# Optimization experiments

Hardware: AMD Instinct MI355X
Metric: run time of the kernel (lower is better)

The kernel has to match this reference:

```python
import jax, jax.numpy as jnp
import numpy as np

NUM_HEADS = 8
DIM_HEAD = 48
SCALE = DIM_HEAD ** -0.5


def setup_inputs() -> dict:
    key = jax.random.key(0)
    k1, k2, k3 = jax.random.split(key, 3)
    B, N, D = 4, 2048, 384
    inner = NUM_HEADS * DIM_HEAD  # 384
    x = jax.random.normal(k1, (B, N, D), dtype=jnp.float32)
    # store weights in [in, out] layout (equivalent to torch Linear W.T)
    Wqkv = jax.random.normal(k2, (D, 3 * inner), dtype=jnp.float32) * (D ** -0.5)
    Wproj = jax.random.normal(k3, (inner, D), dtype=jnp.float32) * (inner ** -0.5)
    bproj = jnp.zeros((D,), dtype=jnp.float32)
    return {"x": x, "Wqkv": Wqkv, "Wproj": Wproj, "bproj": bproj}


def reference(x, Wqkv, Wproj, bproj):
    B, N, D = x.shape
    h, dh = NUM_HEADS, DIM_HEAD
    C = h * dh
    # fused QKV projection (qkv_bias=False)
    qkv = (x @ Wqkv).reshape(B, N, 3, h, dh)
    q = qkv[:, :, 0].transpose(0, 2, 1, 3)  # [B, h, N, dh]
    k = qkv[:, :, 1].transpose(0, 2, 1, 3)
    v = qkv[:, :, 2].transpose(0, 2, 1, 3)
    # naive attention: materialize [B, h, N, N] scores
    sim = jnp.einsum("bhqd,bhkd->bhqk", q, k) * SCALE
    attn = jax.nn.softmax(sim, axis=-1)
    out = jnp.einsum("bhqk,bhkd->bhqd", attn, v)  # [B, h, N, dh]
    out = out.transpose(0, 2, 1, 3).reshape(B, N, C)
    return out @ Wproj + bproj
```

## Files before the change

### kernel.cpp

```cpp
#include <hip/hip_runtime.h>
#include <hip/hip_bf16.h>


typedef _Float16 f16x8 __attribute__((ext_vector_type(8)));
typedef _Float16 f16x4 __attribute__((ext_vector_type(4)));
typedef float    f32x4 __attribute__((ext_vector_type(4)));
typedef float    f32x16 __attribute__((ext_vector_type(16)));

#define QSCL 0.20822035963448658f

__global__ __launch_bounds__(256) void prep(const float4* __restrict__ x,
                                            const float* __restrict__ wq,
                                            const float* __restrict__ wp,
                                            f16x4* __restrict__ xh4,
                                            _Float16* __restrict__ wqt,
                                            _Float16* __restrict__ wpt)
{
    __shared__ _Float16 t[64][65];
    const int blk = blockIdx.x, tid = threadIdx.x;
    if (blk < 144) {
        const float* src; _Float16* dst; int Nn, k0, n0;
        if (blk < 108) {
            src = wq; dst = wqt; Nn = 1152;
            k0 = (blk % 6) * 64; n0 = (blk / 6) * 64;
        } else {
            const int b2 = blk - 108;
            src = wp; dst = wpt; Nn = 384;
            k0 = (b2 % 6) * 64; n0 = (b2 / 6) * 64;
        }
        #pragma unroll
        for (int i = 0; i < 16; i++) {
            const int id = tid + i * 256;
            const int k = id >> 6, n = id & 63;
            t[k][n] = (_Float16)src[(size_t)(k0 + k) * Nn + n0 + n];
        }
        __syncthreads();
        #pragma unroll
        for (int i = 0; i < 16; i++) {
            const int id = tid + i * 256;
            const int n = id >> 6, k = id & 63;
            dst[(size_t)(n0 + n) * 384 + k0 + k] = t[k][n];
        }
    } else {
        const int base = (blk - 144) * 3072;
        #pragma unroll
        for (int r = 0; r < 12; r++) {
            const int j = base + r * 256 + tid;
            const float4 tt = x[j];
            f16x4 h;
            h[0] = (_Float16)tt.x; h[1] = (_Float16)tt.y;
            h[2] = (_Float16)tt.z; h[3] = (_Float16)tt.w;
            xh4[j] = h;
        }
    }
}

__global__ __launch_bounds__(256) void qkv_f16(const _Float16* __restrict__ A,
                                               const _Float16* __restrict__ Bt,
                                               _Float16* __restrict__ qh,
                                               _Float16* __restrict__ kh,
                                               _Float16* __restrict__ vt)
{
    __shared__ _Float16 As[128][72];
    __shared__ _Float16 Bs[64][72];
    const int tid = threadIdx.x;
    const int w = tid >> 6, lane = tid & 63, cl = lane & 15, quad = lane >> 4;
    const int bm = blockIdx.x, bn = blockIdx.y;

    f32x4 acc[2][4];
    const f32x4 z4 = {0.f, 0.f, 0.f, 0.f};
    #pragma unroll
    for (int mi = 0; mi < 2; mi++)
        #pragma unroll
        for (int t = 0; t < 4; t++) acc[mi][t] = z4;

    const int ar = tid >> 3, ac = (tid & 7) * 8;
    const _Float16* Ag = A  + (size_t)(bm * 128 + ar) * 384 + ac;
    const _Float16* Bg = Bt + (size_t)(bn * 64  + ar) * 384 + ac;

    f16x8 pa[4], pb[2];
    #pragma unroll
    for (int j = 0; j < 4; j++) pa[j] = *(const f16x8*)(Ag + (size_t)(32 * j) * 384);
    #pragma unroll
    for (int j = 0; j < 2; j++) pb[j] = *(const f16x8*)(Bg + (size_t)(32 * j) * 384);

    for (int k0 = 0; k0 < 384; k0 += 64) {
        __syncthreads();
        #pragma unroll
        for (int j = 0; j < 4; j++) *(f16x8*)&As[ar + 32 * j][ac] = pa[j];
        #pragma unroll
        for (int j = 0; j < 2; j++) *(f16x8*)&Bs[ar + 32 * j][ac] = pb[j];
        __syncthreads();
        if (k0 + 64 < 384) {
            #pragma unroll
            for (int j = 0; j < 4; j++)
                pa[j] = *(const f16x8*)(Ag + (size_t)(32 * j) * 384 + k0 + 64);
            #pragma unroll
            for (int j = 0; j < 2; j++)
                pb[j] = *(const f16x8*)(Bg + (size_t)(32 * j) * 384 + k0 + 64);
        }
        #pragma unroll
        for (int kh2 = 0; kh2 < 2; kh2++) {
            f16x8 bf[4];
            #pragma unroll
            for (int t = 0; t < 4; t++)
                bf[t] = *(const f16x8*)&Bs[t * 16 + cl][kh2 * 32 + quad * 8];
            #pragma unroll
            for (int mi = 0; mi < 2; mi++) {
                const f16x8 af = *(const f16x8*)&As[w * 32 + mi * 16 + cl][kh2 * 32 + quad * 8];
                #pragma unroll
                for (int t = 0; t < 4; t++)
                    acc[mi][t] = __builtin_amdgcn_mfma_f32_16x16x32_f16(af, bf[t], acc[mi][t], 0, 0, 0);
            }
        }
    }

    const int s = (bn * 64) / 384;
    #pragma unroll
    for (int t = 0; t < 4; t++) {
        const int col  = bn * 64 + t * 16 + cl - s * 384;
        const int head = col / 48, d = col - head * 48;
        #pragma unroll
        for (int mi = 0; mi < 2; mi++) {
            #pragma unroll
            for (int r = 0; r < 4; r++) {
                const int row = bm * 128 + w * 32 + mi * 16 + quad * 4 + r;
                const int b = row >> 11, n = row & 2047;
                const int bh = b * 8 + head;
                const float v = acc[mi][t][r];
                if (s == 0)
                    qh[(size_t)(bh * 2048 + n) * 48 + d] = (_Float16)(v * QSCL);
                else if (s == 1)
                    kh[(size_t)(bh * 2048 + n) * 48 + d] = (_Float16)v;
                else
                    vt[(size_t)(bh * 48 + d) * 2048 + n] = (_Float16)v;
            }
        }
    }
}

__global__ __launch_bounds__(256) void attn_f16(const _Float16* __restrict__ qh,
                                                const _Float16* __restrict__ kh,
                                                const _Float16* __restrict__ vt,
                                                _Float16* __restrict__ ab)
{
    __shared__ _Float16 Ks[64][56];
    __shared__ _Float16 Vts[64][72];
    __shared__ _Float16 Ps[128][72];
    const int tid = threadIdx.x;
    const int w = tid >> 6, lane = tid & 63, ln = lane & 31, h = lane >> 5;
    const int bh = blockIdx.x, qt = blockIdx.y;

    for (int i = tid; i < 16 * 72; i += 256) {
        const int r = 48 + i / 72, c = i - (i / 72) * 72;
        Vts[r][c] = (r == 48) ? (_Float16)1.0f : (_Float16)0.0f;
    }

    f16x8 qf[3];
    {
        const _Float16* qp = qh + (size_t)(bh * 2048 + qt * 128 + w * 32 + ln) * 48 + 8 * h;
        qf[0] = *(const f16x8*)qp;
        qf[1] = *(const f16x8*)(qp + 16);
        qf[2] = *(const f16x8*)(qp + 32);
    }

    f32x16 o0, o1;
    #pragma unroll
    for (int r = 0; r < 16; r++) { o0[r] = 0.f; o1[r] = 0.f; }

    const _Float16* kbase = kh + (size_t)bh * 2048 * 48;
    const _Float16* vbase = vt + (size_t)bh * 48 * 2048;

    const int kr0 = tid / 6,         kc0 = (tid % 6) * 8;
    const int kid1 = tid + 256;
    const int kr1 = kid1 / 6,        kc1 = (kid1 % 6) * 8;
    const int vr0 = tid >> 3,        vc0 = (tid & 7) * 8;
    const int vr1 = (tid + 256) >> 3;
    const _Float16* ks0 = kbase + (size_t)kr0 * 48 + kc0;
    const _Float16* ks1 = kbase + (size_t)kr1 * 48 + kc1;
    const _Float16* vs0 = vbase + (size_t)vr0 * 2048 + vc0;
    const _Float16* vs1 = vbase + (size_t)vr1 * 2048 + vc0;

    f16x8 rk0 = *(const f16x8*)ks0;
    f16x8 rv0 = *(const f16x8*)vs0;
    f16x8 rk1, rv1;
    if (tid < 128) { rk1 = *(const f16x8*)ks1; rv1 = *(const f16x8*)vs1; }

    for (int kt = 0; kt < 2048; kt += 64) {
        __syncthreads();
        *(f16x8*)&Ks[kr0][kc0]  = rk0;
        *(f16x8*)&Vts[vr0][vc0] = rv0;
        if (tid < 128) {
            *(f16x8*)&Ks[kr1][kc1]  = rk1;
            *(f16x8*)&Vts[vr1][vc0] = rv1;
        }
        __syncthreads();
        if (kt + 64 < 2048) {
            rk0 = *(const f16x8*)(ks0 + (size_t)(kt + 64) * 48);
            rv0 = *(const f16x8*)(vs0 + kt + 64);
            if (tid < 128) {
                rk1 = *(const f16x8*)(ks1 + (size_t)(kt + 64) * 48);
                rv1 = *(const f16x8*)(vs1 + kt + 64);
            }
        }

        f32x16 s0, s1;
        #pragma unroll
        for (int r = 0; r < 16; r++) { s0[r] = 0.f; s1[r] = 0.f; }
        #pragma unroll
        for (int i = 0; i < 3; i++) {
            const f16x8 ka0 = *(const f16x8*)&Ks[ln][16 * i + 8 * h];
            s0 = __builtin_amdgcn_mfma_f32_32x32x16_f16(ka0, qf[i], s0, 0, 0, 0);
            const f16x8 ka1 = *(const f16x8*)&Ks[32 + ln][16 * i + 8 * h];
            s1 = __builtin_amdgcn_mfma_f32_32x32x16_f16(ka1, qf[i], s1, 0, 0, 0);
        }

        #pragma unroll
        for (int q = 0; q < 4; q++) {
            f16x4 pk;
            pk[0] = (_Float16)exp2f(s0[4 * q + 0]);
            pk[1] = (_Float16)exp2f(s0[4 * q + 1]);
            pk[2] = (_Float16)exp2f(s0[4 * q + 2]);
            pk[3] = (_Float16)exp2f(s0[4 * q + 3]);
            *(f16x4*)&Ps[w * 32 + ln][8 * q + 4 * h] = pk;
            f16x4 pk1;
            pk1[0] = (_Float16)exp2f(s1[4 * q + 0]);
            pk1[1] = (_Float16)exp2f(s1[4 * q + 1]);
            pk1[2] = (_Float16)exp2f(s1[4 * q + 2]);
            pk1[3] = (_Float16)exp2f(s1[4 * q + 3]);
            *(f16x4*)&Ps[w * 32 + ln][32 + 8 * q + 4 * h] = pk1;
        }

        #pragma unroll
        for (int i = 0; i < 4; i++) {
            const f16x8 pa = *(const f16x8*)&Ps[w * 32 + ln][16 * i + 8 * h];
            const f16x8 v0 = *(const f16x8*)&Vts[ln][16 * i + 8 * h];
            o0 = __builtin_amdgcn_mfma_f32_32x32x16_f16(pa, v0, o0, 0, 0, 0);
            const f16x8 v1 = *(const f16x8*)&Vts[32 + ln][16 * i + 8 * h];
            o1 = __builtin_amdgcn_mfma_f32_32x32x16_f16(pa, v1, o1, 0, 0, 0);
        }
    }

    const int b = bh >> 3, hd = bh & 7;
    #pragma unroll
    for (int r = 0; r < 16; r++) {
        const float lr = __shfl(o1[r], (lane & 32) + 16);
        const float inv = 1.f / lr;
        const int q = qt * 128 + w * 32 + (r & 3) + 8 * (r >> 2) + 4 * h;
        _Float16* orow = ab + (size_t)(b * 2048 + q) * 384 + hd * 48;
        orow[ln] = (_Float16)(o0[r] * inv);
        if (ln < 16) orow[32 + ln] = (_Float16)(o1[r] * inv);
    }
}

__global__ __launch_bounds__(256) void proj_f16(const _Float16* __restrict__ A,
                                                const _Float16* __restrict__ Bt,
                                                const float* __restrict__ bias,
                                                float* __restrict__ out)
{
    __shared__ _Float16 As[64][72];
    __shared__ _Float16 Bs[64][72];
    const int tid = threadIdx.x;
    const int w = tid >> 6, lane = tid & 63, cl = lane & 15, quad = lane >> 4;
    const int bm = blockIdx.x, bn = blockIdx.y;

    f32x4 acc[4];
    const f32x4 z4 = {0.f, 0.f, 0.f, 0.f};
    #pragma unroll
    for (int t = 0; t < 4; t++) acc[t] = z4;

    const int ar = tid >> 3, ac = (tid & 7) * 8;
    const _Float16* Ag = A  + (size_t)(bm * 64 + ar) * 384 + ac;
    const _Float16* Bg = Bt + (size_t)(bn * 64 + ar) * 384 + ac;

    f16x8 pa[2], pb[2];
    #pragma unroll
    for (int j = 0; j < 2; j++) {
        pa[j] = *(const f16x8*)(Ag + (size_t)(32 * j) * 384);
        pb[j] = *(const f16x8*)(Bg + (size_t)(32 * j) * 384);
    }

    for (int k0 = 0; k0 < 384; k0 += 64) {
        __syncthreads();
        #pragma unroll
        for (int j = 0; j < 2; j++) {
            *(f16x8*)&As[ar + 32 * j][ac] = pa[j];
            *(f16x8*)&Bs[ar + 32 * j][ac] = pb[j];
        }
        __syncthreads();
        if (k0 + 64 < 384) {
            #pragma unroll
            for (int j = 0; j < 2; j++) {
                pa[j] = *(const f16x8*)(Ag + (size_t)(32 * j) * 384 + k0 + 64);
                pb[j] = *(const f16x8*)(Bg + (size_t)(32 * j) * 384 + k0 + 64);
            }
        }
        #pragma unroll
        for (int kh2 = 0; kh2 < 2; kh2++) {
            const f16x8 af = *(const f16x8*)&As[w * 16 + cl][kh2 * 32 + quad * 8];
            #pragma unroll
            for (int t = 0; t < 4; t++) {
                const f16x8 bf = *(const f16x8*)&Bs[t * 16 + cl][kh2 * 32 + quad * 8];
                acc[t] = __builtin_amdgcn_mfma_f32_16x16x32_f16(af, bf, acc[t], 0, 0, 0);
            }
        }
    }

    #pragma unroll
    for (int t = 0; t < 4; t++) {
        const int col = bn * 64 + t * 16 + cl;
        const float bv = bias[col];
        #pragma unroll
        for (int r = 0; r < 4; r++) {
            const int row = bm * 64 + w * 16 + quad * 4 + r;
            out[(size_t)row * 384 + col] = acc[t][r] + bv;
        }
    }
}

extern "C" void kernel_launch(void* const* d_in, const int* in_sizes, int n_in,
                              void* d_out, int out_size, void* d_ws, size_t ws_size,
                              hipStream_t stream) {
    const float* x     = (const float*)d_in[0];
    const float* Wqkv  = (const float*)d_in[1];
    const float* Wproj = (const float*)d_in[2];
    const float* bproj = (const float*)d_in[3];
    float* out = (float*)d_out;

    char* ws = (char*)d_ws;
    _Float16* xh     = (_Float16*)(ws + 0);
    _Float16* wqkvt  = (_Float16*)(ws + 6291456);
    _Float16* wprojt = (_Float16*)(ws + 7176192);
    _Float16* qh     = (_Float16*)(ws + 7471104);
    _Float16* kh     = (_Float16*)(ws + 13762560);
    _Float16* vt     = (_Float16*)(ws + 20054016);
    _Float16* ab     = (_Float16*)(ws + 26345472);

    prep<<<400, 256, 0, stream>>>((const float4*)x, Wqkv, Wproj,
                                  (f16x4*)xh, wqkvt, wprojt);
    qkv_f16<<<dim3(64, 18), 256, 0, stream>>>(xh, wqkvt, qh, kh, vt);
    attn_f16<<<dim3(32, 16), 256, 0, stream>>>(qh, kh, vt, ab);
    proj_f16<<<dim3(128, 6), 256, 0, stream>>>(ab, wprojt, bproj, out);
}
```

Before: 154.7 us.

## Fuse x fp16 conversion into QKV GEMM and split attention keys across wave pairs

The prep kernel no longer converts x to fp16. Instead the QKV GEMM loads x as fp32 and converts it while staging into shared memory, which removes a full write and re-read of the fp16 activation copy. The attention kernel now handles 64 queries per block, with two waves per 32-query group each covering half of every 64-key tile. Partial outputs are reduced through a shared-memory union, which doubles the grid to 1024 blocks for better occupancy and latency hiding. The cost is that K/V tiles are re-streamed by twice as many blocks, fp32 A loads double the global load traffic in the GEMM, and there is an extra reduction step at the end of attention.

```diff
diff --git a/kernel.cpp b/kernel.cpp
--- a/kernel.cpp
+++ b/kernel.cpp
@@ -9,53 +9,38 @@
 
 #define QSCL 0.20822035963448658f
 
-__global__ __launch_bounds__(256) void prep(const float4* __restrict__ x,
-                                            const float* __restrict__ wq,
+__global__ __launch_bounds__(256) void prep(const float* __restrict__ wq,
                                             const float* __restrict__ wp,
-                                            f16x4* __restrict__ xh4,
                                             _Float16* __restrict__ wqt,
                                             _Float16* __restrict__ wpt)
 {
     __shared__ _Float16 t[64][65];
     const int blk = blockIdx.x, tid = threadIdx.x;
-    if (blk < 144) {
-        const float* src; _Float16* dst; int Nn, k0, n0;
-        if (blk < 108) {
-            src = wq; dst = wqt; Nn = 1152;
-            k0 = (blk % 6) * 64; n0 = (blk / 6) * 64;
-        } else {
-            const int b2 = blk - 108;
-            src = wp; dst = wpt; Nn = 384;
-            k0 = (b2 % 6) * 64; n0 = (b2 / 6) * 64;
-        }
-        #pragma unroll
-        for (int i = 0; i < 16; i++) {
-            const int id = tid + i * 256;
-            const int k = id >> 6, n = id & 63;
-            t[k][n] = (_Float16)src[(size_t)(k0 + k) * Nn + n0 + n];
-        }
-        __syncthreads();
-        #pragma unroll
-        for (int i = 0; i < 16; i++) {
-            const int id = tid + i * 256;
-            const int n = id >> 6, k = id & 63;
-            dst[(size_t)(n0 + n) * 384 + k0 + k] = t[k][n];
-        }
+    const float* src; _Float16* dst; int Nn, k0, n0;
+    if (blk < 108) {
+        src = wq; dst = wqt; Nn = 1152;
+        k0 = (blk % 6) * 64; n0 = (blk / 6) * 64;
     } else {
-        const int base = (blk - 144) * 3072;
-        #pragma unroll
-        for (int r = 0; r < 12; r++) {
-            const int j = base + r * 256 + tid;
-            const float4 tt = x[j];
-            f16x4 h;
-            h[0] = (_Float16)tt.x; h[1] = (_Float16)tt.y;
-            h[2] = (_Float16)tt.z; h[3] = (_Float16)tt.w;
-            xh4[j] = h;
-        }
-    }
-}
-
-__global__ __launch_bounds__(256) void qkv_f16(const _Float16* __restrict__ A,
+        const int b2 = blk - 108;
+        src = wp; dst = wpt; Nn = 384;
+        k0 = (b2 % 6) * 64; n0 = (b2 / 6) * 64;
+    }
+    #pragma unroll
+    for (int i = 0; i < 16; i++) {
+        const int id = tid + i * 256;
+        const int k = id >> 6, n = id & 63;
+        t[k][n] = (_Float16)src[(size_t)(k0 + k) * Nn + n0 + n];
+    }
+    __syncthreads();
+    #pragma unroll
+    for (int i = 0; i < 16; i++) {
+        const int id = tid + i * 256;
+        const int n = id >> 6, k = id & 63;
+        dst[(size_t)(n0 + n) * 384 + k0 + k] = t[k][n];
+    }
+}
+
+__global__ __launch_bounds__(256) void qkv_f16(const float* __restrict__ X,
                                                const _Float16* __restrict__ Bt,
                                                _Float16* __restrict__ qh,
                                                _Float16* __restrict__ kh,
@@ -75,26 +60,39 @@
         for (int t = 0; t < 4; t++) acc[mi][t] = z4;
 
     const int ar = tid >> 3, ac = (tid & 7) * 8;
-    const _Float16* Ag = A  + (size_t)(bm * 128 + ar) * 384 + ac;
+    const float*    Ag = X  + (size_t)(bm * 128 + ar) * 384 + ac;
     const _Float16* Bg = Bt + (size_t)(bn * 64  + ar) * 384 + ac;
 
-    f16x8 pa[4], pb[2];
-    #pragma unroll
-    for (int j = 0; j < 4; j++) pa[j] = *(const f16x8*)(Ag + (size_t)(32 * j) * 384);
+    float4 pa0[4], pa1[4];
+    f16x8 pb[2];
+    #pragma unroll
+    for (int j = 0; j < 4; j++) {
+        pa0[j] = *(const float4*)(Ag + (size_t)(32 * j) * 384);
+        pa1[j] = *(const float4*)(Ag + (size_t)(32 * j) * 384 + 4);
+    }
     #pragma unroll
     for (int j = 0; j < 2; j++) pb[j] = *(const f16x8*)(Bg + (size_t)(32 * j) * 384);
 
     for (int k0 = 0; k0 < 384; k0 += 64) {
         __syncthreads();
         #pragma unroll
-        for (int j = 0; j < 4; j++) *(f16x8*)&As[ar + 32 * j][ac] = pa[j];
+        for (int j = 0; j < 4; j++) {
+            f16x8 hh;
+            hh[0] = (_Float16)pa0[j].x; hh[1] = (_Float16)pa0[j].y;
+            hh[2] = (_Float16)pa0[j].z; hh[3] = (_Float16)pa0[j].w;
+            hh[4] = (_Float16)pa1[j].x; hh[5] = (_Float16)pa1[j].y;
+            hh[6] = (_Float16)pa1[j].z; hh[7] = (_Float16)pa1[j].w;
+            *(f16x8*)&As[ar + 32 * j][ac] = hh;
+        }
         #pragma unroll
         for (int j = 0; j < 2; j++) *(f16x8*)&Bs[ar + 32 * j][ac] = pb[j];
         __syncthreads();
         if (k0 + 64 < 384) {
             #pragma unroll
-            for (int j = 0; j < 4; j++)
-                pa[j] = *(const f16x8*)(Ag + (size_t)(32 * j) * 384 + k0 + 64);
+            for (int j = 0; j < 4; j++) {
+                pa0[j] = *(const float4*)(Ag + (size_t)(32 * j) * 384 + k0 + 64);
+                pa1[j] = *(const float4*)(Ag + (size_t)(32 * j) * 384 + k0 + 68);
+            }
             #pragma unroll
             for (int j = 0; j < 2; j++)
                 pb[j] = *(const f16x8*)(Bg + (size_t)(32 * j) * 384 + k0 + 64);
@@ -139,26 +137,34 @@
     }
 }
 
+union AttnSmem {
+    struct {
+        _Float16 Ks[64][56];
+        _Float16 Vts[64][72];
+        _Float16 Ps[64][72];
+    } a;
+    float mb[2][32][50];
+};
+
 __global__ __launch_bounds__(256) void attn_f16(const _Float16* __restrict__ qh,
                                                 const _Float16* __restrict__ kh,
                                                 const _Float16* __restrict__ vt,
                                                 _Float16* __restrict__ ab)
 {
-    __shared__ _Float16 Ks[64][56];
-    __shared__ _Float16 Vts[64][72];
-    __shared__ _Float16 Ps[128][72];
+    __shared__ AttnSmem sm;
     const int tid = threadIdx.x;
     const int w = tid >> 6, lane = tid & 63, ln = lane & 31, h = lane >> 5;
+    const int pair = w >> 1, half = w & 1;
     const int bh = blockIdx.x, qt = blockIdx.y;
 
     for (int i = tid; i < 16 * 72; i += 256) {
         const int r = 48 + i / 72, c = i - (i / 72) * 72;
-        Vts[r][c] = (r == 48) ? (_Float16)1.0f : (_Float16)0.0f;
+        sm.a.Vts[r][c] = (r == 48) ? (_Float16)1.0f : (_Float16)0.0f;
     }
 
     f16x8 qf[3];
     {
-        const _Float16* qp = qh + (size_t)(bh * 2048 + qt * 128 + w * 32 + ln) * 48 + 8 * h;
+        const _Float16* qp = qh + (size_t)(bh * 2048 + qt * 64 + pair * 32 + ln) * 48 + 8 * h;
         qf[0] = *(const f16x8*)qp;
         qf[1] = *(const f16x8*)(qp + 16);
         qf[2] = *(const f16x8*)(qp + 32);
@@ -188,11 +194,11 @@
 
     for (int kt = 0; kt < 2048; kt += 64) {
         __syncthreads();
-        *(f16x8*)&Ks[kr0][kc0]  = rk0;
-        *(f16x8*)&Vts[vr0][vc0] = rv0;
+        *(f16x8*)&sm.a.Ks[kr0][kc0]  = rk0;
+        *(f16x8*)&sm.a.Vts[vr0][vc0] = rv0;
         if (tid < 128) {
-            *(f16x8*)&Ks[kr1][kc1]  = rk1;
-            *(f16x8*)&Vts[vr1][vc0] = rv1;
+            *(f16x8*)&sm.a.Ks[kr1][kc1]  = rk1;
+            *(f16x8*)&sm.a.Vts[vr1][vc0] = rv1;
         }
         __syncthreads();
         if (kt + 64 < 2048) {
@@ -204,52 +210,59 @@
             }
         }
 
-        f32x16 s0, s1;
-        #pragma unroll
-        for (int r = 0; r < 16; r++) { s0[r] = 0.f; s1[r] = 0.f; }
+        f32x16 s;
+        #pragma unroll
+        for (int r = 0; r < 16; r++) s[r] = 0.f;
         #pragma unroll
         for (int i = 0; i < 3; i++) {
-            const f16x8 ka0 = *(const f16x8*)&Ks[ln][16 * i + 8 * h];
-            s0 = __builtin_amdgcn_mfma_f32_32x32x16_f16(ka0, qf[i], s0, 0, 0, 0);
-            const f16x8 ka1 = *(const f16x8*)&Ks[32 + ln][16 * i + 8 * h];
-            s1 = __builtin_amdgcn_mfma_f32_32x32x16_f16(ka1, qf[i], s1, 0, 0, 0);
+            const f16x8 ka = *(const f16x8*)&sm.a.Ks[half * 32 + ln][16 * i + 8 * h];
+            s = __builtin_amdgcn_mfma_f32_32x32x16_f16(ka, qf[i], s, 0, 0, 0);
         }
 
         #pragma unroll
         for (int q = 0; q < 4; q++) {
             f16x4 pk;
-            pk[0] = (_Float16)exp2f(s0[4 * q + 0]);
-            pk[1] = (_Float16)exp2f(s0[4 * q + 1]);
-            pk[2] = (_Float16)exp2f(s0[4 * q + 2]);
-            pk[3] = (_Float16)exp2f(s0[4 * q + 3]);
-            *(f16x4*)&Ps[w * 32 + ln][8 * q + 4 * h] = pk;
-            f16x4 pk1;
-            pk1[0] = (_Float16)exp2f(s1[4 * q + 0]);
-            pk1[1] = (_Float16)exp2f(s1[4 * q + 1]);
-            pk1[2] = (_Float16)exp2f(s1[4 * q + 2]);
-            pk1[3] = (_Float16)exp2f(s1[4 * q + 3]);
-            *(f16x4*)&Ps[w * 32 + ln][32 + 8 * q + 4 * h] = pk1;
-        }
-
-        #pragma unroll
-        for (int i = 0; i < 4; i++) {
-            const f16x8 pa = *(const f16x8*)&Ps[w * 32 + ln][16 * i + 8 * h];
-            const f16x8 v0 = *(const f16x8*)&Vts[ln][16 * i + 8 * h];
+            pk[0] = (_Float16)exp2f(s[4 * q + 0]);
+            pk[1] = (_Float16)exp2f(s[4 * q + 1]);
+            pk[2] = (_Float16)exp2f(s[4 * q + 2]);
+            pk[3] = (_Float16)exp2f(s[4 * q + 3]);
+            *(f16x4*)&sm.a.Ps[pair * 32 + ln][half * 32 + 8 * q + 4 * h] = pk;
+        }
+
+        #pragma unroll
+        for (int i = 0; i < 2; i++) {
+            const f16x8 pa = *(const f16x8*)&sm.a.Ps[pair * 32 + ln][half * 32 + 16 * i + 8 * h];
+            const f16x8 v0 = *(const f16x8*)&sm.a.Vts[ln][half * 32 + 16 * i + 8 * h];
             o0 = __builtin_amdgcn_mfma_f32_32x32x16_f16(pa, v0, o0, 0, 0, 0);
-            const f16x8 v1 = *(const f16x8*)&Vts[32 + ln][16 * i + 8 * h];
+            const f16x8 v1 = *(const f16x8*)&sm.a.Vts[32 + ln][half * 32 + 16 * i + 8 * h];
             o1 = __builtin_amdgcn_mfma_f32_32x32x16_f16(pa, v1, o1, 0, 0, 0);
         }
     }
 
-    const int b = bh >> 3, hd = bh & 7;
-    #pragma unroll
-    for (int r = 0; r < 16; r++) {
-        const float lr = __shfl(o1[r], (lane & 32) + 16);
-        const float inv = 1.f / lr;
-        const int q = qt * 128 + w * 32 + (r & 3) + 8 * (r >> 2) + 4 * h;
-        _Float16* orow = ab + (size_t)(b * 2048 + q) * 384 + hd * 48;
-        orow[ln] = (_Float16)(o0[r] * inv);
-        if (ln < 16) orow[32 + ln] = (_Float16)(o1[r] * inv);
+    __syncthreads();
+    if (half == 1) {
+        #pragma unroll
+        for (int r = 0; r < 16; r++) {
+            const int row = (r & 3) + 8 * (r >> 2) + 4 * h;
+            sm.mb[pair][row][ln] = o0[r];
+            if (ln < 17) sm.mb[pair][row][32 + ln] = o1[r];
+        }
+    }
+    __syncthreads();
+    if (half == 0) {
+        const int b = bh >> 3, hd = bh & 7;
+        #pragma unroll
+        for (int r = 0; r < 16; r++) {
+            const int row = (r & 3) + 8 * (r >> 2) + 4 * h;
+            o0[r] += sm.mb[pair][row][ln];
+            if (ln < 17) o1[r] += sm.mb[pair][row][32 + ln];
+            const float lr = __shfl(o1[r], (lane & 32) + 16);
+            const float inv = 1.f / lr;
+            const int q = qt * 64 + pair * 32 + row;
+            _Float16* orow = ab + (size_t)(b * 2048 + q) * 384 + hd * 48;
+            orow[ln] = (_Float16)(o0[r] * inv);
+            if (ln < 16) orow[32 + ln] = (_Float16)(o1[r] * inv);
+        }
     }
 }
 
@@ -328,17 +341,15 @@
     float* out = (float*)d_out;
 
     char* ws = (char*)d_ws;
-    _Float16* xh     = (_Float16*)(ws + 0);
-    _Float16* wqkvt  = (_Float16*)(ws + 6291456);
-    _Float16* wprojt = (_Float16*)(ws + 7176192);
-    _Float16* qh     = (_Float16*)(ws + 7471104);
-    _Float16* kh     = (_Float16*)(ws + 13762560);
-    _Float16* vt     = (_Float16*)(ws + 20054016);
-    _Float16* ab     = (_Float16*)(ws + 26345472);
-
-    prep<<<400, 256, 0, stream>>>((const float4*)x, Wqkv, Wproj,
-                                  (f16x4*)xh, wqkvt, wprojt);
-    qkv_f16<<<dim3(64, 18), 256, 0, stream>>>(xh, wqkvt, qh, kh, vt);
-    attn_f16<<<dim3(32, 16), 256, 0, stream>>>(qh, kh, vt, ab);
+    _Float16* wqkvt  = (_Float16*)(ws + 0);
+    _Float16* wprojt = (_Float16*)(ws + 884736);
+    _Float16* qh     = (_Float16*)(ws + 1179648);
+    _Float16* kh     = (_Float16*)(ws + 7471104);
+    _Float16* vt     = (_Float16*)(ws + 13762560);
+    _Float16* ab     = (_Float16*)(ws + 20054016);
+
+    prep<<<144, 256, 0, stream>>>(Wqkv, Wproj, wqkvt, wprojt);
+    qkv_f16<<<dim3(64, 18), 256, 0, stream>>>(x, wqkvt, qh, kh, vt);
+    attn_f16<<<dim3(32, 32), 256, 0, stream>>>(qh, kh, vt, ab);
     proj_f16<<<dim3(128, 6), 256, 0, stream>>>(ab, wprojt, bproj, out);
 }
```

Result: slower. 221.9 us (+43.5%).

## Fuse x fp16 conversion into QKV GEMM and stage V transpose via LDS

Applied to the files above, without the earlier changes.

Drops the separate fp32-to-fp16 pass over x from the prep kernel. The QKV GEMM now loads fp32 x directly and converts it while writing to shared memory, which removes one full write and re-read of a 6 MB fp16 buffer. The V output tiles are also transposed through a shared-memory union buffer, so V^T is written with coalesced 16-byte stores instead of scattered 2-byte stores. The cost is that each GEMM block reads x twice as many bytes, since x is now fp32, and this load is repeated by all 18 column blocks.

```diff
diff --git a/kernel.cpp b/kernel.cpp
--- a/kernel.cpp
+++ b/kernel.cpp
@@ -9,60 +9,49 @@
 
 #define QSCL 0.20822035963448658f
 
-__global__ __launch_bounds__(256) void prep(const float4* __restrict__ x,
-                                            const float* __restrict__ wq,
+__global__ __launch_bounds__(256) void prep(const float* __restrict__ wq,
                                             const float* __restrict__ wp,
-                                            f16x4* __restrict__ xh4,
                                             _Float16* __restrict__ wqt,
                                             _Float16* __restrict__ wpt)
 {
     __shared__ _Float16 t[64][65];
     const int blk = blockIdx.x, tid = threadIdx.x;
-    if (blk < 144) {
-        const float* src; _Float16* dst; int Nn, k0, n0;
-        if (blk < 108) {
-            src = wq; dst = wqt; Nn = 1152;
-            k0 = (blk % 6) * 64; n0 = (blk / 6) * 64;
-        } else {
-            const int b2 = blk - 108;
-            src = wp; dst = wpt; Nn = 384;
-            k0 = (b2 % 6) * 64; n0 = (b2 / 6) * 64;
-        }
-        #pragma unroll
-        for (int i = 0; i < 16; i++) {
-            const int id = tid + i * 256;
-            const int k = id >> 6, n = id & 63;
-            t[k][n] = (_Float16)src[(size_t)(k0 + k) * Nn + n0 + n];
-        }
-        __syncthreads();
-        #pragma unroll
-        for (int i = 0; i < 16; i++) {
-            const int id = tid + i * 256;
-            const int n = id >> 6, k = id & 63;
-            dst[(size_t)(n0 + n) * 384 + k0 + k] = t[k][n];
-        }
+    const float* src; _Float16* dst; int Nn, k0, n0;
+    if (blk < 108) {
+        src = wq; dst = wqt; Nn = 1152;
+        k0 = (blk % 6) * 64; n0 = (blk / 6) * 64;
     } else {
-        const int base = (blk - 144) * 3072;
-        #pragma unroll
-        for (int r = 0; r < 12; r++) {
-            const int j = base + r * 256 + tid;
-            const float4 tt = x[j];
-            f16x4 h;
-            h[0] = (_Float16)tt.x; h[1] = (_Float16)tt.y;
-            h[2] = (_Float16)tt.z; h[3] = (_Float16)tt.w;
-            xh4[j] = h;
-        }
-    }
-}
-
-__global__ __launch_bounds__(256) void qkv_f16(const _Float16* __restrict__ A,
+        const int b2 = blk - 108;
+        src = wp; dst = wpt; Nn = 384;
+        k0 = (b2 % 6) * 64; n0 = (b2 / 6) * 64;
+    }
+    #pragma unroll
+    for (int i = 0; i < 16; i++) {
+        const int id = tid + i * 256;
+        const int k = id >> 6, n = id & 63;
+        t[k][n] = (_Float16)src[(size_t)(k0 + k) * Nn + n0 + n];
+    }
+    __syncthreads();
+    #pragma unroll
+    for (int i = 0; i < 16; i++) {
+        const int id = tid + i * 256;
+        const int n = id >> 6, k = id & 63;
+        dst[(size_t)(n0 + n) * 384 + k0 + k] = t[k][n];
+    }
+}
+
+union QkvSmem {
+    struct { _Float16 As[128][72]; _Float16 Bs[64][72]; } g;
+    _Float16 Ts[64][136];
+};
+
+__global__ __launch_bounds__(256) void qkv_f16(const float* __restrict__ X,
                                                const _Float16* __restrict__ Bt,
                                                _Float16* __restrict__ qh,
                                                _Float16* __restrict__ kh,
                                                _Float16* __restrict__ vt)
 {
-    __shared__ _Float16 As[128][72];
-    __shared__ _Float16 Bs[64][72];
+    __shared__ QkvSmem sm;
     const int tid = threadIdx.x;
     const int w = tid >> 6, lane = tid & 63, cl = lane & 15, quad = lane >> 4;
     const int bm = blockIdx.x, bn = blockIdx.y;
@@ -75,26 +64,39 @@
         for (int t = 0; t < 4; t++) acc[mi][t] = z4;
 
     const int ar = tid >> 3, ac = (tid & 7) * 8;
-    const _Float16* Ag = A  + (size_t)(bm * 128 + ar) * 384 + ac;
+    const float*    Ag = X  + (size_t)(bm * 128 + ar) * 384 + ac;
     const _Float16* Bg = Bt + (size_t)(bn * 64  + ar) * 384 + ac;
 
-    f16x8 pa[4], pb[2];
-    #pragma unroll
-    for (int j = 0; j < 4; j++) pa[j] = *(const f16x8*)(Ag + (size_t)(32 * j) * 384);
+    float4 pa0[4], pa1[4];
+    f16x8 pb[2];
+    #pragma unroll
+    for (int j = 0; j < 4; j++) {
+        pa0[j] = *(const float4*)(Ag + (size_t)(32 * j) * 384);
+        pa1[j] = *(const float4*)(Ag + (size_t)(32 * j) * 384 + 4);
+    }
     #pragma unroll
     for (int j = 0; j < 2; j++) pb[j] = *(const f16x8*)(Bg + (size_t)(32 * j) * 384);
 
     for (int k0 = 0; k0 < 384; k0 += 64) {
         __syncthreads();
         #pragma unroll
-        for (int j = 0; j < 4; j++) *(f16x8*)&As[ar + 32 * j][ac] = pa[j];
-        #pragma unroll
-        for (int j = 0; j < 2; j++) *(f16x8*)&Bs[ar + 32 * j][ac] = pb[j];
+        for (int j = 0; j < 4; j++) {
+            f16x8 hh;
+            hh[0] = (_Float16)pa0[j].x; hh[1] = (_Float16)pa0[j].y;
+            hh[2] = (_Float16)pa0[j].z; hh[3] = (_Float16)pa0[j].w;
+            hh[4] = (_Float16)pa1[j].x; hh[5] = (_Float16)pa1[j].y;
+            hh[6] = (_Float16)pa1[j].z; hh[7] = (_Float16)pa1[j].w;
+            *(f16x8*)&sm.g.As[ar + 32 * j][ac] = hh;
+        }
+        #pragma unroll
+        for (int j = 0; j < 2; j++) *(f16x8*)&sm.g.Bs[ar + 32 * j][ac] = pb[j];
         __syncthreads();
         if (k0 + 64 < 384) {
             #pragma unroll
-            for (int j = 0; j < 4; j++)
-                pa[j] = *(const f16x8*)(Ag + (size_t)(32 * j) * 384 + k0 + 64);
+            for (int j = 0; j < 4; j++) {
+                pa0[j] = *(const float4*)(Ag + (size_t)(32 * j) * 384 + k0 + 64);
+                pa1[j] = *(const float4*)(Ag + (size_t)(32 * j) * 384 + k0 + 68);
+            }
             #pragma unroll
             for (int j = 0; j < 2; j++)
                 pb[j] = *(const f16x8*)(Bg + (size_t)(32 * j) * 384 + k0 + 64);
@@ -104,10 +106,10 @@
             f16x8 bf[4];
             #pragma unroll
             for (int t = 0; t < 4; t++)
-                bf[t] = *(const f16x8*)&Bs[t * 16 + cl][kh2 * 32 + quad * 8];
+                bf[t] = *(const f16x8*)&sm.g.Bs[t * 16 + cl][kh2 * 32 + quad * 8];
             #pragma unroll
             for (int mi = 0; mi < 2; mi++) {
-                const f16x8 af = *(const f16x8*)&As[w * 32 + mi * 16 + cl][kh2 * 32 + quad * 8];
+                const f16x8 af = *(const f16x8*)&sm.g.As[w * 32 + mi * 16 + cl][kh2 * 32 + quad * 8];
                 #pragma unroll
                 for (int t = 0; t < 4; t++)
                     acc[mi][t] = __builtin_amdgcn_mfma_f32_16x16x32_f16(af, bf[t], acc[mi][t], 0, 0, 0);
@@ -116,24 +118,48 @@
     }
 
     const int s = (bn * 64) / 384;
-    #pragma unroll
-    for (int t = 0; t < 4; t++) {
-        const int col  = bn * 64 + t * 16 + cl - s * 384;
-        const int head = col / 48, d = col - head * 48;
-        #pragma unroll
-        for (int mi = 0; mi < 2; mi++) {
-            #pragma unroll
-            for (int r = 0; r < 4; r++) {
-                const int row = bm * 128 + w * 32 + mi * 16 + quad * 4 + r;
-                const int b = row >> 11, n = row & 2047;
-                const int bh = b * 8 + head;
-                const float v = acc[mi][t][r];
-                if (s == 0)
-                    qh[(size_t)(bh * 2048 + n) * 48 + d] = (_Float16)(v * QSCL);
-                else if (s == 1)
-                    kh[(size_t)(bh * 2048 + n) * 48 + d] = (_Float16)v;
-                else
-                    vt[(size_t)(bh * 48 + d) * 2048 + n] = (_Float16)v;
+    if (s == 2) {
+        __syncthreads();
+        #pragma unroll
+        for (int t = 0; t < 4; t++)
+            #pragma unroll
+            for (int mi = 0; mi < 2; mi++)
+                #pragma unroll
+                for (int r = 0; r < 4; r++)
+                    sm.Ts[t * 16 + cl][w * 32 + mi * 16 + quad * 4 + r] =
+                        (_Float16)acc[mi][t][r];
+        __syncthreads();
+        const int colbase = bn * 64 - 768;
+        const int b  = (bm * 128) >> 11;
+        const int n0 = (bm * 128) & 2047;
+        #pragma unroll
+        for (int i = 0; i < 4; i++) {
+            const int c = i * 256 + tid;
+            const int col = c >> 4, nc = c & 15;
+            const int gcol = colbase + col;
+            const int head = gcol / 48, d = gcol - head * 48;
+            const int bh = b * 8 + head;
+            *(f16x8*)&vt[(size_t)(bh * 48 + d) * 2048 + n0 + nc * 8] =
+                *(const f16x8*)&sm.Ts[col][nc * 8];
+        }
+    } else {
+        #pragma unroll
+        for (int t = 0; t < 4; t++) {
+            const int col  = bn * 64 + t * 16 + cl - s * 384;
+            const int head = col / 48, d = col - head * 48;
+            #pragma unroll
+            for (int mi = 0; mi < 2; mi++) {
+                #pragma unroll
+                for (int r = 0; r < 4; r++) {
+                    const int row = bm * 128 + w * 32 + mi * 16 + quad * 4 + r;
+                    const int b = row >> 11, n = row & 2047;
+                    const int bh = b * 8 + head;
+                    const float v = acc[mi][t][r];
+                    if (s == 0)
+                        qh[(size_t)(bh * 2048 + n) * 48 + d] = (_Float16)(v * QSCL);
+                    else
+                        kh[(size_t)(bh * 2048 + n) * 48 + d] = (_Float16)v;
+                }
             }
         }
     }
@@ -328,17 +354,15 @@
     float* out = (float*)d_out;
 
     char* ws = (char*)d_ws;
-    _Float16* xh     = (_Float16*)(ws + 0);
-    _Float16* wqkvt  = (_Float16*)(ws + 6291456);
-    _Float16* wprojt = (_Float16*)(ws + 7176192);
-    _Float16* qh     = (_Float16*)(ws + 7471104);
-    _Float16* kh     = (_Float16*)(ws + 13762560);
-    _Float16* vt     = (_Float16*)(ws + 20054016);
-    _Float16* ab     = (_Float16*)(ws + 26345472);
-
-    prep<<<400, 256, 0, stream>>>((const float4*)x, Wqkv, Wproj,
-                                  (f16x4*)xh, wqkvt, wprojt);
-    qkv_f16<<<dim3(64, 18), 256, 0, stream>>>(xh, wqkvt, qh, kh, vt);
+    _Float16* wqkvt  = (_Float16*)(ws + 0);
+    _Float16* wprojt = (_Float16*)(ws + 884736);
+    _Float16* qh     = (_Float16*)(ws + 1179648);
+    _Float16* kh     = (_Float16*)(ws + 7471104);
+    _Float16* vt     = (_Float16*)(ws + 13762560);
+    _Float16* ab     = (_Float16*)(ws + 20054016);
+
+    prep<<<144, 256, 0, stream>>>(Wqkv, Wproj, wqkvt, wprojt);
+    qkv_f16<<<dim3(64, 18), 256, 0, stream>>>(x, wqkvt, qh, kh, vt);
     attn_f16<<<dim3(32, 16), 256, 0, stream>>>(qh, kh, vt, ab);
     proj_f16<<<dim3(128, 6), 256, 0, stream>>>(ab, wprojt, bproj, out);
 }
```

Measured after the change: 152.4 us. About the same (-1.5%).
